# Kernel optimization log

Measured on AMD Instinct MI355X. Metric: run time of the kernel, lower is better.

The kernel has to match this reference:

```python
import jax, jax.numpy as jnp
import numpy as np

N_NODES = 50000
N_EDGES = 600000
N_GRAPHS = 2048
EMB = 128
N_LAYERS = 3
ATOM_FEATS, ATOM_VOCAB = 9, 100
BOND_FEATS, BOND_VOCAB, BOND_DIM = 3, 8, 3


def setup_inputs() -> dict:
    key = jax.random.key(0)
    ks = jax.random.split(key, 10)
    x = jax.random.randint(ks[0], (N_NODES, ATOM_FEATS), 0, ATOM_VOCAB)
    edge_index = jax.random.randint(ks[1], (2, N_EDGES), 0, N_NODES)
    edge_attr = jax.random.randint(ks[2], (N_EDGES, BOND_FEATS), 0, BOND_VOCAB)
    batch = jnp.sort(jax.random.randint(ks[3], (N_NODES,), 0, N_GRAPHS))
    s = 1.0 / np.sqrt(EMB).astype(np.float32)
    atom_emb = jax.random.normal(ks[4], (ATOM_FEATS, ATOM_VOCAB, EMB), jnp.float32) * 0.1
    bond_emb = jax.random.normal(ks[5], (N_LAYERS, BOND_FEATS, BOND_VOCAB, BOND_DIM), jnp.float32) * 0.1
    W = jax.random.normal(ks[6], (N_LAYERS, BOND_DIM, EMB, EMB), jnp.float32) * s
    b = jnp.zeros((N_LAYERS, BOND_DIM, EMB), jnp.float32)
    fc1_w = jax.random.normal(ks[7], (EMB, EMB), jnp.float32) * s
    fc1_b = jnp.zeros((EMB,), jnp.float32)
    fc2_w = jax.random.normal(ks[8], (EMB, 1), jnp.float32) * s
    fc2_b = jnp.zeros((1,), jnp.float32)
    return dict(x=x, edge_index=edge_index, edge_attr=edge_attr, batch=batch,
                atom_emb=atom_emb, bond_emb=bond_emb, W=W, b=b,
                fc1_w=fc1_w, fc1_b=fc1_b, fc2_w=fc2_w, fc2_b=fc2_b)


def reference(x, edge_index, edge_attr, batch, atom_emb, bond_emb, W, b,
              fc1_w, fc1_b, fc2_w, fc2_b):
    src, dst = edge_index[0], edge_index[1]
    n = x.shape[0]
    # AtomEncoder: sum of per-column embedding lookups -> [N, EMB]
    h = atom_emb[0][x[:, 0]]
    for c in range(1, ATOM_FEATS):
        h = h + atom_emb[c][x[:, c]]
    for layer in range(N_LAYERS):
        # BondEncoder: [E, BOND_DIM] edge weights (one scalar channel per conv)
        ew = bond_emb[layer, 0][edge_attr[:, 0]]
        for c in range(1, BOND_FEATS):
            ew = ew + bond_emb[layer, c][edge_attr[:, c]]
        # Three parallel GCNConv(normalize=False): linear, gather src, edge-weight, scatter-add to dst
        msg = jnp.zeros((edge_index.shape[1], EMB), h.dtype)
        for k in range(BOND_DIM):
            xw = h @ W[layer, k]              # [N, EMB]
            msg = msg + ew[:, k:k + 1] * xw[src]   # [E, EMB]
        agg = jax.ops.segment_sum(msg, dst, num_segments=n)
        hn = agg + jnp.sum(b[layer], axis=0)  # sum of the three conv biases
        if layer < N_LAYERS - 1:
            hn = jax.nn.relu(hn)              # dropout is identity at eval
        h = hn + h                            # residual
    # global_mean_pool
    sums = jax.ops.segment_sum(h, batch, num_segments=N_GRAPHS)
    counts = jax.ops.segment_sum(jnp.ones((n,), h.dtype), batch, num_segments=N_GRAPHS)
    hg = sums / jnp.maximum(counts, 1.0)[:, None]
    return (hg @ fc1_w + fc1_b) @ fc2_w + fc2_b   # [N_GRAPHS, 1]
```

## Files before the change

kernel.cpp:

```cpp
#include <hip/hip_runtime.h>

#define N_NODES 50000
#define N_EDGES 600000
#define N_GRAPHS 2048
#define EMB 128
#define TDIM 384
#define TS_LD 392
#define HN (N_NODES * EMB)
#define SCAN_NB ((N_NODES + 255) / 256)
#define DEG_STRIDE 32
#define GROWS 64

#define PRE_ATOM_NB 8334
#define PRE_HIST_NB 1563
#define PRE_WCONV_NB 384
#define PRE_GB_NB 131

typedef __attribute__((ext_vector_type(8))) short bf16x8;
typedef __attribute__((ext_vector_type(4))) float f32x4;
#define MFMA_BF16(a, b, c) __builtin_amdgcn_mfma_f32_16x16x32_bf16(a, b, c, 0, 0, 0)

#define AS1 __attribute__((address_space(1)))
#define AS3 __attribute__((address_space(3)))
__device__ inline void gl_lds16(const void* g, void* l) {
  __builtin_amdgcn_global_load_lds((const AS1 void*)g, (AS3 void*)l, 16, 0, 0);
}

__device__ inline unsigned short f2bf(float f) {
  unsigned int u = __float_as_uint(f);
  u += 0x7fffu + ((u >> 16) & 1u);
  return (unsigned short)(u >> 16);
}
__device__ inline float bf2f(unsigned short b) {
  return __uint_as_float(((unsigned int)b) << 16);
}
__device__ inline bf16x8 pack8(float4 lo, float4 hi) {
  bf16x8 r;
  r[0] = (short)f2bf(lo.x); r[1] = (short)f2bf(lo.y);
  r[2] = (short)f2bf(lo.z); r[3] = (short)f2bf(lo.w);
  r[4] = (short)f2bf(hi.x); r[5] = (short)f2bf(hi.y);
  r[6] = (short)f2bf(hi.z); r[7] = (short)f2bf(hi.w);
  return r;
}

__global__ __launch_bounds__(384) void k_pre(const int* __restrict__ x,
                                             const float* __restrict__ atom_emb,
                                             unsigned short* __restrict__ h_bf,
                                             const int* __restrict__ ei,
                                             int* __restrict__ degP,
                                             int* __restrict__ rank,
                                             const float* __restrict__ W,
                                             unsigned short* __restrict__ wt,
                                             const int* __restrict__ batch,
                                             int* __restrict__ gs) {
  __shared__ float sb[6 * 1280];
  int blk = blockIdx.x;
  if (blk < PRE_ATOM_NB) {
    const int wv = threadIdx.x >> 6;
    const int lane = threadIdx.x & 63;
    int n = blk * 6 + wv;
    if (n < N_NODES) {
      const int nu = __builtin_amdgcn_readfirstlane(n);
      const int* xr = x + nu * 9;
      int ix[9];
#pragma unroll
      for (int c = 0; c < 9; ++c) ix[c] = xr[c];
      float* wbase = sb + wv * 1280;
      const int half = lane >> 5;
      const int sub16 = lane & 31;
#pragma unroll
      for (int j = 0; j < 4; ++j) {
        int c = 2 * j + half;
        const float* g = atom_emb + (size_t)(c * 100 + ix[c]) * EMB + sub16 * 4;
        gl_lds16(g, wbase + j * 256);
      }
      {
        const float* g = atom_emb + (size_t)(8 * 100 + ix[8]) * EMB + sub16 * 4;
        gl_lds16(g, wbase + 1024);
      }
      asm volatile("s_waitcnt vmcnt(0)" ::: "memory");
      float2 acc = {0.f, 0.f};
#pragma unroll
      for (int c = 0; c < 9; ++c) {
        float2 v = *(const float2*)(wbase + c * 128 + lane * 2);
        acc.x += v.x; acc.y += v.y;
      }
      *(ushort2*)(h_bf + (size_t)nu * EMB + lane * 2) = ushort2{f2bf(acc.x), f2bf(acc.y)};
    }
    return;
  }
  blk -= PRE_ATOM_NB;
  if (blk < PRE_HIST_NB) {
    int e = blk * 384 + threadIdx.x;
    if (e < N_EDGES) {
      int d = ei[N_EDGES + e];
      rank[e] = atomicAdd(&degP[(size_t)d * DEG_STRIDE], 1);
    }
    return;
  }
  blk -= PRE_HIST_NB;
  if (blk < PRE_WCONV_NB) {
    int layer = blk >> 7, c = blk & 127, k = threadIdx.x;
    float v = W[(((layer * 3 + (k >> 7)) * 128) + (k & 127)) * 128 + c];
    wt[(size_t)blk * 384 + k] = f2bf(v);
    return;
  }
  blk -= PRE_WCONV_NB;
  {
    int i = blk * 384 + threadIdx.x;
    if (i < N_NODES) {
      int b = batch[i];
      int bp = (i == 0) ? -1 : batch[i - 1];
      for (int g = bp + 1; g <= b; ++g) gs[g] = i;
      if (i == N_NODES - 1) {
        for (int g = b + 1; g <= N_GRAPHS; ++g) gs[g] = N_NODES;
      }
    }
  }
}

__global__ __launch_bounds__(256) void k_scan_a(const int* __restrict__ degP,
                                                int* __restrict__ row_start,
                                                int* __restrict__ partials) {
  __shared__ int s[256];
  const int tid = threadIdx.x;
  const int i = blockIdx.x * 256 + tid;
  int v = (i < N_NODES) ? degP[(size_t)i * DEG_STRIDE] : 0;
  s[tid] = v;
  __syncthreads();
  for (int off = 1; off < 256; off <<= 1) {
    int t = (tid >= off) ? s[tid - off] : 0;
    __syncthreads();
    s[tid] += t;
    __syncthreads();
  }
  if (i < N_NODES) row_start[i] = s[tid] - v;
  if (tid == 255) partials[blockIdx.x] = s[255];
}

__global__ __launch_bounds__(256) void k_scan_b(int* __restrict__ partials,
                                                int* __restrict__ row_start) {
  __shared__ int s[256];
  const int tid = threadIdx.x;
  int v = (tid < SCAN_NB) ? partials[tid] : 0;
  s[tid] = v;
  __syncthreads();
  for (int off = 1; off < 256; off <<= 1) {
    int t = (tid >= off) ? s[tid - off] : 0;
    __syncthreads();
    s[tid] += t;
    __syncthreads();
  }
  if (tid < SCAN_NB) partials[tid] = s[tid] - v;
  if (tid == 255) row_start[N_NODES] = s[255];
}

__global__ __launch_bounds__(256) void k_scan_c(int* __restrict__ row_start,
                                                const int* __restrict__ partials) {
  const int i = blockIdx.x * 256 + threadIdx.x;
  if (i < N_NODES) row_start[i] += partials[blockIdx.x];
}

__global__ __launch_bounds__(256) void k_scatter(const int* __restrict__ ei,
                                                 const int* __restrict__ ea,
                                                 const int* __restrict__ rank,
                                                 const int* __restrict__ row_start,
                                                 int2* __restrict__ sorted_se) {
  int e = blockIdx.x * 256 + threadIdx.x;
  if (e >= N_EDGES) return;
  int src = ei[e], dst = ei[N_EDGES + e];
  int pos = row_start[dst] + rank[e];
  int eap = ea[e * 3 + 0] | (ea[e * 3 + 1] << 3) | (ea[e * 3 + 2] << 6);
  sorted_se[pos] = int2{src, eap};
}

__global__ __launch_bounds__(256) void k_agg(const int2* __restrict__ sorted_se,
                                             const int* __restrict__ row_start,
                                             const float* __restrict__ bl,
                                             const unsigned short* __restrict__ h_bf,
                                             unsigned short* __restrict__ t_bf) {
  __shared__ float4 combo[512];
  for (int c = threadIdx.x; c < 512; c += 256) {
    int a0 = c & 7, a1 = (c >> 3) & 7, a2 = (c >> 6) & 7;
    combo[c] = float4{bl[a0 * 3 + 0] + bl[24 + a1 * 3 + 0] + bl[48 + a2 * 3 + 0],
                      bl[a0 * 3 + 1] + bl[24 + a1 * 3 + 1] + bl[48 + a2 * 3 + 1],
                      bl[a0 * 3 + 2] + bl[24 + a1 * 3 + 2] + bl[48 + a2 * 3 + 2], 0.f};
  }
  __syncthreads();
  const int node = blockIdx.x * 16 + (threadIdx.x >> 4);
  const int sub = threadIdx.x & 15;
  const int beg = row_start[node], end = row_start[node + 1];
  float4 l0 = {0.f, 0.f, 0.f, 0.f}, h0 = l0;
  float4 l1 = l0, h1 = l0;
  float4 l2 = l0, h2 = l0;
  int e = beg;
  const int full_end = beg + ((end - beg) & ~7);
  for (; e < full_end; e += 8) {
    int2 se[8];
#pragma unroll
    for (int j = 0; j < 8; ++j) se[j] = sorted_se[e + j];
    bf16x8 u[8];
#pragma unroll
    for (int j = 0; j < 8; ++j)
      u[j] = *(const bf16x8*)(h_bf + (size_t)se[j].x * EMB + sub * 8);
#pragma unroll
    for (int j = 0; j < 8; ++j) {
      float4 w = combo[se[j].y];
      float4 vlo = {bf2f((unsigned short)u[j][0]), bf2f((unsigned short)u[j][1]),
                    bf2f((unsigned short)u[j][2]), bf2f((unsigned short)u[j][3])};
      float4 vhi = {bf2f((unsigned short)u[j][4]), bf2f((unsigned short)u[j][5]),
                    bf2f((unsigned short)u[j][6]), bf2f((unsigned short)u[j][7])};
      l0 += vlo * w.x; h0 += vhi * w.x;
      l1 += vlo * w.y; h1 += vhi * w.y;
      l2 += vlo * w.z; h2 += vhi * w.z;
    }
  }
  if (e < end) {
    int2 se[8];
#pragma unroll
    for (int j = 0; j < 8; ++j) {
      int idx = e + j;
      se[j] = sorted_se[idx < end ? idx : end - 1];
    }
    bf16x8 u[8];
#pragma unroll
    for (int j = 0; j < 8; ++j)
      u[j] = *(const bf16x8*)(h_bf + (size_t)se[j].x * EMB + sub * 8);
#pragma unroll
    for (int j = 0; j < 8; ++j) {
      float4 w = (e + j < end) ? combo[se[j].y] : float4{0.f, 0.f, 0.f, 0.f};
      float4 vlo = {bf2f((unsigned short)u[j][0]), bf2f((unsigned short)u[j][1]),
                    bf2f((unsigned short)u[j][2]), bf2f((unsigned short)u[j][3])};
      float4 vhi = {bf2f((unsigned short)u[j][4]), bf2f((unsigned short)u[j][5]),
                    bf2f((unsigned short)u[j][6]), bf2f((unsigned short)u[j][7])};
      l0 += vlo * w.x; h0 += vhi * w.x;
      l1 += vlo * w.y; h1 += vhi * w.y;
      l2 += vlo * w.z; h2 += vhi * w.z;
    }
  }
  size_t base = (size_t)node * TDIM + sub * 8;
  *(bf16x8*)(t_bf + base)       = pack8(l0, h0);
  *(bf16x8*)(t_bf + base + 128) = pack8(l1, h1);
  *(bf16x8*)(t_bf + base + 256) = pack8(l2, h2);
}

__global__ __launch_bounds__(512) void k_gemm(const unsigned short* __restrict__ t_bf,
                                              const unsigned short* __restrict__ wt,
                                              const float* __restrict__ bl,
                                              const unsigned short* __restrict__ h_in_bf,
                                              unsigned short* __restrict__ h_out_bf,
                                              int do_relu) {
  __shared__ unsigned short ts[GROWS * TS_LD];
  const int nb = blockIdx.x * GROWS;
  for (int i = threadIdx.x; i < GROWS * 48; i += 512) {
    int r = i / 48, cc = i % 48;
    bf16x8 v = {};
    int row = nb + r;
    if (row < N_NODES) v = *(const bf16x8*)(t_bf + (size_t)row * TDIM + cc * 8);
    *(bf16x8*)(ts + r * TS_LD + cc * 8) = v;
  }
  __syncthreads();

  const int wv = threadIdx.x >> 6;
  const int lane = threadIdx.x & 63;
  const int m = lane & 15;
  const int kq = lane >> 4;
  const int c = wv * 16 + m;

  const unsigned short* pB = wt + (size_t)c * TDIM + kq * 8;
  bf16x8 B[12];
#pragma unroll
  for (int kc = 0; kc < 12; ++kc) B[kc] = *(const bf16x8*)(pB + kc * 32);

  const float bias = bl[c] + bl[128 + c] + bl[256 + c];

#pragma unroll
  for (int rt = 0; rt < 4; ++rt) {
    const unsigned short* pA = ts + (rt * 16 + m) * TS_LD + kq * 8;
    bf16x8 A[12];
#pragma unroll
    for (int kc = 0; kc < 12; ++kc) A[kc] = *(const bf16x8*)(pA + kc * 32);
    f32x4 acc = {0.f, 0.f, 0.f, 0.f};
#pragma unroll
    for (int kc = 0; kc < 12; ++kc) acc = MFMA_BF16(A[kc], B[kc], acc);
#pragma unroll
    for (int r = 0; r < 4; ++r) {
      int row = nb + rt * 16 + kq * 4 + r;
      if (row < N_NODES) {
        size_t idx = (size_t)row * EMB + c;
        float v = acc[r] + bias;
        if (do_relu) v = fmaxf(v, 0.f);
        float hn = bf2f(h_in_bf[idx]) + v;
        h_out_bf[idx] = f2bf(hn);
      }
    }
  }
}

__global__ __launch_bounds__(128) void k_head(const unsigned short* __restrict__ h_bf,
                                              const int* __restrict__ gs,
                                              const float* __restrict__ fc1_w,
                                              const float* __restrict__ fc1_b,
                                              const float* __restrict__ fc2_w,
                                              const float* __restrict__ fc2_b,
                                              float* __restrict__ out) {
  __shared__ float hg[EMB];
  __shared__ float red[EMB];
  int g = blockIdx.x, e = threadIdx.x;
  int ns = gs[g], ne = gs[g + 1];
  float acc = 0.f;
  for (int n = ns; n < ne; ++n) acc += bf2f(h_bf[(size_t)n * EMB + e]);
  float cnt = fmaxf((float)(ne - ns), 1.f);
  hg[e] = acc / cnt;
  __syncthreads();
  float a2 = fc1_b[e];
  for (int j = 0; j < EMB; ++j) a2 += hg[j] * fc1_w[j * EMB + e];
  red[e] = a2 * fc2_w[e];
  __syncthreads();
  for (int s = 64; s > 0; s >>= 1) {
    if (e < s) red[e] += red[e + s];
    __syncthreads();
  }
  if (e == 0) out[g] = red[0] + fc2_b[0];
}

extern "C" void kernel_launch(void* const* d_in, const int* in_sizes, int n_in,
                              void* d_out, int out_size, void* d_ws, size_t ws_size,
                              hipStream_t stream) {
  const int*   x        = (const int*)d_in[0];
  const int*   ei       = (const int*)d_in[1];
  const int*   ea       = (const int*)d_in[2];
  const int*   batch    = (const int*)d_in[3];
  const float* atom_emb = (const float*)d_in[4];
  const float* bond_emb = (const float*)d_in[5];
  const float* W        = (const float*)d_in[6];
  const float* b        = (const float*)d_in[7];
  const float* fc1_w    = (const float*)d_in[8];
  const float* fc1_b    = (const float*)d_in[9];
  const float* fc2_w    = (const float*)d_in[10];
  const float* fc2_b    = (const float*)d_in[11];
  float* out = (float*)d_out;

  char* p = (char*)d_ws;
  auto alloc = [&](size_t bytes) { char* r = p; p += (bytes + 255) & ~(size_t)255; return r; };
  unsigned short* h0_bf      = (unsigned short*)alloc((size_t)HN * 2);
  unsigned short* h1_bf      = (unsigned short*)alloc((size_t)HN * 2);
  unsigned short* t_bf       = (unsigned short*)alloc((size_t)N_NODES * TDIM * 2);
  unsigned short* wt         = (unsigned short*)alloc((size_t)3 * 128 * TDIM * 2);
  int*            gs         = (int*)alloc((size_t)(N_GRAPHS + 1) * 4);
  int*            degP       = (int*)alloc((size_t)N_NODES * DEG_STRIDE * 4);
  int*            rank       = (int*)alloc((size_t)N_EDGES * 4);
  int*            row_start  = (int*)alloc((size_t)(N_NODES + 1) * 4);
  int*            partials   = (int*)alloc(256 * 4);
  int2*           sorted_se  = (int2*)alloc((size_t)(N_EDGES + 8) * 8);

  hipMemsetAsync(degP, 0, (size_t)N_NODES * DEG_STRIDE * sizeof(int), stream);
  const int pre_blocks = PRE_ATOM_NB + PRE_HIST_NB + PRE_WCONV_NB + PRE_GB_NB;
  k_pre<<<pre_blocks, 384, 0, stream>>>(x, atom_emb, h0_bf, ei, degP, rank, W, wt, batch, gs);
  k_scan_a<<<SCAN_NB, 256, 0, stream>>>(degP, row_start, partials);
  k_scan_b<<<1, 256, 0, stream>>>(partials, row_start);
  k_scan_c<<<SCAN_NB, 256, 0, stream>>>(row_start, partials);
  k_scatter<<<(N_EDGES + 255) / 256, 256, 0, stream>>>(ei, ea, rank, row_start, sorted_se);

  unsigned short* hib = h0_bf;
  unsigned short* hob = h1_bf;
  const int gemm_blocks = (N_NODES + GROWS - 1) / GROWS;
  for (int layer = 0; layer < 3; ++layer) {
    k_agg<<<N_NODES / 16, 256, 0, stream>>>(sorted_se, row_start, bond_emb + layer * 72,
                                            hib, t_bf);
    k_gemm<<<gemm_blocks, 512, 0, stream>>>(
        t_bf, wt + (size_t)layer * 128 * TDIM, b + layer * 3 * EMB,
        hib, hob, layer < 2 ? 1 : 0);
    unsigned short* tb = hib; hib = hob; hob = tb;
  }

  k_head<<<N_GRAPHS, 128, 0, stream>>>(hib, gs, fc1_w, fc1_b, fc2_w, fc2_b, out);
}
```

Measured before the change: 343.7 us.

## Replace global-atomic CSR build with two-pass LDS bucket radix sort by destination

Builds the destination-sorted edge list (CSR) with a two-level counting sort instead of global atomics on padded degree counters. A coarse pass histograms edges into 256-node buckets in LDS per 2048-edge block, a single-block scan computes bucket offsets, and a scatter writes into a temporary buffer. A fine pass per bucket then sorts by the low 8 bits in LDS and writes row_start and sorted_se. This removes the memset, the contended global atomics and the three scan kernels, but adds an extra pass over a temporary edge buffer and a serial per-thread scan over about 293 block counts.

```diff
diff --git a/kernel.cpp b/kernel.cpp
--- a/kernel.cpp
+++ b/kernel.cpp
@@ -7,12 +7,13 @@
 #define TDIM 384
 #define TS_LD 392
 #define HN (N_NODES * EMB)
-#define SCAN_NB ((N_NODES + 255) / 256)
-#define DEG_STRIDE 32
 #define GROWS 64
 
+#define EPB 2048
+#define NBLKA ((N_EDGES + EPB - 1) / EPB)
+#define NCOARSE ((N_NODES + 255) / 256)
+
 #define PRE_ATOM_NB 8334
-#define PRE_HIST_NB 1563
 #define PRE_WCONV_NB 384
 #define PRE_GB_NB 131
 
@@ -46,9 +47,6 @@
 __global__ __launch_bounds__(384) void k_pre(const int* __restrict__ x,
                                              const float* __restrict__ atom_emb,
                                              unsigned short* __restrict__ h_bf,
-                                             const int* __restrict__ ei,
-                                             int* __restrict__ degP,
-                                             int* __restrict__ rank,
                                              const float* __restrict__ W,
                                              unsigned short* __restrict__ wt,
                                              const int* __restrict__ batch,
@@ -90,15 +88,6 @@
     return;
   }
   blk -= PRE_ATOM_NB;
-  if (blk < PRE_HIST_NB) {
-    int e = blk * 384 + threadIdx.x;
-    if (e < N_EDGES) {
-      int d = ei[N_EDGES + e];
-      rank[e] = atomicAdd(&degP[(size_t)d * DEG_STRIDE], 1);
-    }
-    return;
-  }
-  blk -= PRE_HIST_NB;
   if (blk < PRE_WCONV_NB) {
     int layer = blk >> 7, c = blk & 127, k = threadIdx.x;
     float v = W[(((layer * 3 + (k >> 7)) * 128) + (k & 127)) * 128 + c];
@@ -119,59 +108,101 @@
   }
 }
 
-__global__ __launch_bounds__(256) void k_scan_a(const int* __restrict__ degP,
-                                                int* __restrict__ row_start,
-                                                int* __restrict__ partials) {
+__global__ __launch_bounds__(256) void k_cnt(const int* __restrict__ ei,
+                                             int* __restrict__ ghist) {
+  __shared__ int h[256];
+  const int t = threadIdx.x;
+  h[t] = 0;
+  __syncthreads();
+  const int base = blockIdx.x * EPB;
+#pragma unroll
+  for (int k = 0; k < 8; ++k) {
+    int e = base + k * 256 + t;
+    if (e < N_EDGES) atomicAdd(&h[ei[N_EDGES + e] >> 8], 1);
+  }
+  __syncthreads();
+  if (t < NCOARSE) ghist[(size_t)t * NBLKA + blockIdx.x] = h[t];
+}
+
+__global__ __launch_bounds__(256) void k_sscan(int* __restrict__ ghist,
+                                               int* __restrict__ bucket_base,
+                                               int* __restrict__ row_start) {
   __shared__ int s[256];
-  const int tid = threadIdx.x;
-  const int i = blockIdx.x * 256 + tid;
-  int v = (i < N_NODES) ? degP[(size_t)i * DEG_STRIDE] : 0;
-  s[tid] = v;
+  const int t = threadIdx.x;
+  int sum = 0;
+  if (t < NCOARSE) {
+    int* row = ghist + (size_t)t * NBLKA;
+    for (int b = 0; b < NBLKA; ++b) { int v = row[b]; row[b] = sum; sum += v; }
+  }
+  s[t] = sum;
   __syncthreads();
   for (int off = 1; off < 256; off <<= 1) {
-    int t = (tid >= off) ? s[tid - off] : 0;
+    int v = (t >= off) ? s[t - off] : 0;
     __syncthreads();
-    s[tid] += t;
+    s[t] += v;
     __syncthreads();
   }
-  if (i < N_NODES) row_start[i] = s[tid] - v;
-  if (tid == 255) partials[blockIdx.x] = s[255];
-}
-
-__global__ __launch_bounds__(256) void k_scan_b(int* __restrict__ partials,
-                                                int* __restrict__ row_start) {
+  if (t < NCOARSE) bucket_base[t] = s[t] - sum;
+  if (t == 0) { bucket_base[NCOARSE] = N_EDGES; row_start[N_NODES] = N_EDGES; }
+}
+
+__global__ __launch_bounds__(256) void k_coarse(const int* __restrict__ ei,
+                                                const int* __restrict__ ea,
+                                                const int* __restrict__ ghist,
+                                                const int* __restrict__ bucket_base,
+                                                int2* __restrict__ tmp) {
+  __shared__ int cnt[256];
+  const int t = threadIdx.x;
+  cnt[t] = 0;
+  __syncthreads();
+  const int base = blockIdx.x * EPB;
+#pragma unroll
+  for (int k = 0; k < 8; ++k) {
+    int e = base + k * 256 + t;
+    if (e < N_EDGES) {
+      int dst = ei[N_EDGES + e];
+      int d = dst >> 8;
+      int r = atomicAdd(&cnt[d], 1);
+      int pos = bucket_base[d] + ghist[(size_t)d * NBLKA + blockIdx.x] + r;
+      int eap = ea[e * 3 + 0] | (ea[e * 3 + 1] << 3) | (ea[e * 3 + 2] << 6);
+      tmp[pos] = int2{dst | (eap << 16), ei[e]};
+    }
+  }
+}
+
+__global__ __launch_bounds__(256) void k_fine(const int2* __restrict__ tmp,
+                                              const int* __restrict__ bucket_base,
+                                              int* __restrict__ row_start,
+                                              int2* __restrict__ sorted_se) {
+  __shared__ int h[256];
   __shared__ int s[256];
-  const int tid = threadIdx.x;
-  int v = (tid < SCAN_NB) ? partials[tid] : 0;
-  s[tid] = v;
+  __shared__ int ex[256];
+  const int t = threadIdx.x;
+  const int d = blockIdx.x;
+  const int b0 = bucket_base[d], b1 = bucket_base[d + 1];
+  h[t] = 0;
+  __syncthreads();
+  for (int i = b0 + t; i < b1; i += 256) atomicAdd(&h[tmp[i].x & 255], 1);
+  __syncthreads();
+  s[t] = h[t];
   __syncthreads();
   for (int off = 1; off < 256; off <<= 1) {
-    int t = (tid >= off) ? s[tid - off] : 0;
+    int v = (t >= off) ? s[t - off] : 0;
     __syncthreads();
-    s[tid] += t;
+    s[t] += v;
     __syncthreads();
   }
-  if (tid < SCAN_NB) partials[tid] = s[tid] - v;
-  if (tid == 255) row_start[N_NODES] = s[255];
-}
-
-__global__ __launch_bounds__(256) void k_scan_c(int* __restrict__ row_start,
-                                                const int* __restrict__ partials) {
-  const int i = blockIdx.x * 256 + threadIdx.x;
-  if (i < N_NODES) row_start[i] += partials[blockIdx.x];
-}
-
-__global__ __launch_bounds__(256) void k_scatter(const int* __restrict__ ei,
-                                                 const int* __restrict__ ea,
-                                                 const int* __restrict__ rank,
-                                                 const int* __restrict__ row_start,
-                                                 int2* __restrict__ sorted_se) {
-  int e = blockIdx.x * 256 + threadIdx.x;
-  if (e >= N_EDGES) return;
-  int src = ei[e], dst = ei[N_EDGES + e];
-  int pos = row_start[dst] + rank[e];
-  int eap = ea[e * 3 + 0] | (ea[e * 3 + 1] << 3) | (ea[e * 3 + 2] << 6);
-  sorted_se[pos] = int2{src, eap};
+  ex[t] = s[t] - h[t];
+  int node = d * 256 + t;
+  if (node < N_NODES) row_start[node] = b0 + ex[t];
+  h[t] = 0;
+  __syncthreads();
+  for (int i = b0 + t; i < b1; i += 256) {
+    int2 r = tmp[i];
+    int f = r.x & 255;
+    int pos = b0 + ex[f] + atomicAdd(&h[f], 1);
+    sorted_se[pos] = int2{r.y, (r.x >> 16) & 511};
+  }
 }
 
 __global__ __launch_bounds__(256) void k_agg(const int2* __restrict__ sorted_se,
@@ -348,19 +379,18 @@
   unsigned short* t_bf       = (unsigned short*)alloc((size_t)N_NODES * TDIM * 2);
   unsigned short* wt         = (unsigned short*)alloc((size_t)3 * 128 * TDIM * 2);
   int*            gs         = (int*)alloc((size_t)(N_GRAPHS + 1) * 4);
-  int*            degP       = (int*)alloc((size_t)N_NODES * DEG_STRIDE * 4);
-  int*            rank       = (int*)alloc((size_t)N_EDGES * 4);
   int*            row_start  = (int*)alloc((size_t)(N_NODES + 1) * 4);
-  int*            partials   = (int*)alloc(256 * 4);
+  int*            ghist      = (int*)alloc((size_t)NCOARSE * NBLKA * 4);
+  int*            bucket_base= (int*)alloc((size_t)(NCOARSE + 1) * 4);
+  int2*           tmp_se     = (int2*)alloc((size_t)N_EDGES * 8);
   int2*           sorted_se  = (int2*)alloc((size_t)(N_EDGES + 8) * 8);
 
-  hipMemsetAsync(degP, 0, (size_t)N_NODES * DEG_STRIDE * sizeof(int), stream);
-  const int pre_blocks = PRE_ATOM_NB + PRE_HIST_NB + PRE_WCONV_NB + PRE_GB_NB;
-  k_pre<<<pre_blocks, 384, 0, stream>>>(x, atom_emb, h0_bf, ei, degP, rank, W, wt, batch, gs);
-  k_scan_a<<<SCAN_NB, 256, 0, stream>>>(degP, row_start, partials);
-  k_scan_b<<<1, 256, 0, stream>>>(partials, row_start);
-  k_scan_c<<<SCAN_NB, 256, 0, stream>>>(row_start, partials);
-  k_scatter<<<(N_EDGES + 255) / 256, 256, 0, stream>>>(ei, ea, rank, row_start, sorted_se);
+  const int pre_blocks = PRE_ATOM_NB + PRE_WCONV_NB + PRE_GB_NB;
+  k_pre<<<pre_blocks, 384, 0, stream>>>(x, atom_emb, h0_bf, W, wt, batch, gs);
+  k_cnt<<<NBLKA, 256, 0, stream>>>(ei, ghist);
+  k_sscan<<<1, 256, 0, stream>>>(ghist, bucket_base, row_start);
+  k_coarse<<<NBLKA, 256, 0, stream>>>(ei, ea, ghist, bucket_base, tmp_se);
+  k_fine<<<NCOARSE, 256, 0, stream>>>(tmp_se, bucket_base, row_start, sorted_se);
 
   unsigned short* hib = h0_bf;
   unsigned short* hob = h1_bf;
```

Measured after the change: 358.3 us. +4.2%, slower.
